# Kernel tuning notes

Hardware: AMD Instinct MI355X
Metric: run time of the kernel (lower is better)

## Reference

```python
import jax, jax.numpy as jnp
import numpy as np

N_NODES = 100000
N_EDGES = 1000000
N_GRAPHS = 2048
IN_DIM, HIDDEN, OUT_DIM = 5, 64, 128


def setup_inputs() -> dict:
    key = jax.random.key(0)
    ks = jax.random.split(key, 12)
    x = jax.random.normal(ks[0], (N_NODES, IN_DIM), dtype=jnp.float32)
    edge_index = jax.random.randint(ks[1], (2, N_EDGES), 0, N_NODES, dtype=jnp.int64)
    batch = jnp.sort(jax.random.randint(ks[2], (N_NODES,), 0, N_GRAPHS, dtype=jnp.int64))
    def lin(k, fan_in, fan_out):
        bound = 1.0 / np.sqrt(fan_in)
        kw, kb = jax.random.split(k)
        W = jax.random.uniform(kw, (fan_in, fan_out), jnp.float32, -bound, bound)
        b = jax.random.uniform(kb, (fan_out,), jnp.float32, -bound, bound)
        return W, b
    W1, b1 = lin(ks[3], IN_DIM, HIDDEN)
    W2, b2 = lin(ks[4], HIDDEN, HIDDEN)
    W3, b3 = lin(ks[5], HIDDEN, HIDDEN)
    W4, b4 = lin(ks[6], HIDDEN, OUT_DIM)
    return {"x": x, "edge_index": edge_index, "batch": batch,
            "W1": W1, "b1": b1, "W2": W2, "b2": b2,
            "W3": W3, "b3": b3, "W4": W4, "b4": b4}


def _gcn_conv(x, W, b, src, dst, norm, n):
    # h = x W; message from src, scaled by symmetric norm, scattered to dst
    h = x @ W                                   # [N, F]
    msg = h[src] * norm[:, None]                # [E+N, F] gather
    agg = jax.ops.segment_sum(msg, dst, num_segments=n)  # scatter-add
    return agg + b


def reference(x, edge_index, batch, W1, b1, W2, b2, W3, b3, W4, b4):
    n = x.shape[0]
    loop = jnp.arange(n, dtype=edge_index.dtype)
    # GCN with self-loops: src -> dst aggregation, D^-1/2 A_hat D^-1/2 norm
    src = jnp.concatenate([edge_index[0], loop])
    dst = jnp.concatenate([edge_index[1], loop])
    deg = jax.ops.segment_sum(jnp.ones_like(dst, dtype=x.dtype), dst, num_segments=n)
    dinv = jnp.where(deg > 0, jax.lax.rsqrt(jnp.maximum(deg, 1.0)), 0.0)
    norm = dinv[src] * dinv[dst]                # [E+N]

    h = jax.nn.relu(_gcn_conv(x, W1, b1, src, dst, norm, n))
    h = jax.nn.relu(_gcn_conv(h, W2, b2, src, dst, norm, n))

    # global mean pool per graph
    sums = jax.ops.segment_sum(h, batch, num_segments=N_GRAPHS)      # [G, F]
    cnts = jax.ops.segment_sum(jnp.ones((n,), h.dtype), batch, num_segments=N_GRAPHS)
    pooled = sums / jnp.maximum(cnts, 1.0)[:, None]

    # MLP head
    z = jax.nn.relu(pooled @ W3 + b3)
    return z @ W4 + b4
```

## Files before the change

kernel.cpp:

```cpp
#include <hip/hip_runtime.h>
#include <hip/hip_fp16.h>

#define N_NODES  100000
#define N_EDGES  1000000
#define N_GRAPHS 2048
#define IN_DIM   5
#define HIDDEN   64
#define OUT_DIM  128
#define CAP      32
#define NA       512
#define PART     256
#define NBIN     391
#define CAPBIN   4096
#define LSTR     72

typedef _Float16 f16x8 __attribute__((ext_vector_type(8)));
typedef float    f32x4 __attribute__((ext_vector_type(4)));


__global__ void __launch_bounds__(256) k_part2(
        const int* __restrict__ src, const int* __restrict__ dst,
        const int* __restrict__ batch, int* __restrict__ gcursor,
        int* __restrict__ epart, int* __restrict__ gs) {
    __shared__ int h[NBIN];
    __shared__ int off[NBIN];
    int t = threadIdx.x, b = blockIdx.x;

    int gid = b * 256 + t;
    if (gid < N_NODES) {
        int bi = batch[gid];
        int bp = (gid == 0) ? -1 : batch[gid - 1];
        for (int g = bp + 1; g <= bi; g++) gs[g] = gid;
        if (gid == N_NODES - 1)
            for (int g = bi + 1; g <= N_GRAPHS; g++) gs[g] = N_NODES;
    }

    for (int i = t; i < NBIN; i += 256) h[i] = 0;
    __syncthreads();
    for (int e = b * 256 + t; e < N_EDGES; e += NA * 256)
        atomicAdd(&h[dst[e] >> 8], 1);
    __syncthreads();
    for (int i = t; i < NBIN; i += 256) {
        int c = h[i];
        int base = c ? atomicAdd(&gcursor[i], c) : 0;
        off[i] = i * CAPBIN + base;
    }
    __syncthreads();
    for (int e = b * 256 + t; e < N_EDGES; e += NA * 256) {
        int d = dst[e];
        int bin = d >> 8;
        int pos = atomicAdd(&off[bin], 1);
        if (pos < (bin + 1) * CAPBIN)
            epart[pos] = ((d & (PART - 1)) << 17) | src[e];
    }
}

__global__ void __launch_bounds__(256) k_build(
        const int* __restrict__ epart, const int* __restrict__ bincnt,
        const float* __restrict__ x, int* __restrict__ cnt, int* __restrict__ bkt,
        float* __restrict__ dinv, __half* __restrict__ xs) {
    __shared__ int lcnt[PART];
    __shared__ int lrows[PART * CAP];
    int t = threadIdx.x, b = blockIdx.x;
    int base = b * PART;
    for (int i = t; i < PART; i += 256) lcnt[i] = 0;
    __syncthreads();
    int estart = b * CAPBIN;
    int eend = estart + min(bincnt[b], CAPBIN);
    for (int i = estart + t; i < eend; i += 256) {
        int ed = epart[i];
        int ln = ed >> 17;
        int c = atomicAdd(&lcnt[ln], 1);
        if (c < CAP) lrows[ln * CAP + c] = ed & 0x1FFFF;
    }
    __syncthreads();
    int gbase = base * CAP;
    int lim = min(PART * CAP, N_NODES * CAP - gbase);
    for (int i = t; i < lim; i += 256) bkt[gbase + i] = lrows[i];
    for (int n = t; n < PART; n += 256) {
        int g = base + n;
        if (g < N_NODES) {
            int c = lcnt[n];
            cnt[g] = c;
            float d = rsqrtf(1.0f + (float)c);
            dinv[g] = d;
            union { __half h[8]; float4 f4; } u;
#pragma unroll
            for (int k = 0; k < 8; k++)
                u.h[k] = __float2half((k < IN_DIM) ? x[g * IN_DIM + k] * d : 0.0f);
            ((float4*)xs)[g] = u.f4;
        }
    }
}

__global__ void __launch_bounds__(256) k_g5l12(
        const int* __restrict__ cnt, const int* __restrict__ bkt,
        const __half* __restrict__ xs,
        const float* __restrict__ W1, const float* __restrict__ b1,
        const float* __restrict__ W2, const float* __restrict__ dinv,
        __half* __restrict__ hs2h) {
    __shared__ _Float16 lh1[64 * LSTR];
    __shared__ _Float16 lw2[64 * LSTR];
    __shared__ float la5[64][8];
    int tid = threadIdx.x;
    int w = tid >> 6, l = tid & 63;
    int nodeBase = blockIdx.x * 64;

#pragma unroll
    for (int i = 0; i < 16; i++) {
        int idx = tid + i * 256;
        int k = idx >> 6, n = idx & 63;
        lw2[n * LSTR + k] = (_Float16)W2[k * HIDDEN + n];
    }

    {
        int g4 = l >> 2, l4 = l & 3;
        int ln = w * 16 + g4;
        int g = nodeBase + ln;
        float s0 = 0.f, s1 = 0.f, s2 = 0.f, s3 = 0.f;
        float s4 = 0.f, s5 = 0.f, s6 = 0.f, s7 = 0.f;
        if (g < N_NODES) {
            const float4* XS4 = (const float4*)xs;
            int len = min(cnt[g], CAP);
            const int* row = bkt + (size_t)g * CAP;
#define XACC(r) { const __half2* hp_ = (const __half2*)&(r);                   \
            float2 u0_ = __half22float2(hp_[0]), u1_ = __half22float2(hp_[1]); \
            float2 u2_ = __half22float2(hp_[2]), u3_ = __half22float2(hp_[3]); \
            s0 += u0_.x; s1 += u0_.y; s2 += u1_.x; s3 += u1_.y;                \
            s4 += u2_.x; s5 += u2_.y; s6 += u3_.x; s7 += u3_.y; }
            int e = l4;
            for (; e + 4 < len; e += 8) {
                float4 r0 = XS4[row[e]];
                float4 r1 = XS4[row[e + 4]];
                XACC(r0); XACC(r1);
            }
            if (e < len) { float4 r0 = XS4[row[e]]; XACC(r0); }
            if (l4 == 0) { float4 rs = XS4[g]; XACC(rs); }
#undef XACC
        }
#pragma unroll
        for (int m = 1; m <= 2; m <<= 1) {
            s0 += __shfl_xor(s0, m); s1 += __shfl_xor(s1, m);
            s2 += __shfl_xor(s2, m); s3 += __shfl_xor(s3, m);
            s4 += __shfl_xor(s4, m); s5 += __shfl_xor(s5, m);
            s6 += __shfl_xor(s6, m); s7 += __shfl_xor(s7, m);
        }
        if (l4 == 0) {
            float d = (g < N_NODES) ? dinv[g] : 0.f;
            la5[ln][0] = s0 * d; la5[ln][1] = s1 * d;
            la5[ln][2] = s2 * d; la5[ln][3] = s3 * d;
            la5[ln][4] = s4 * d; la5[ln][5] = s5 * d;
            la5[ln][6] = s6 * d; la5[ln][7] = s7 * d;
        }
    }

    int f = l;
    for (int i = 0; i < 16; i++) {
        int ln = w * 16 + i;
        float t1 = b1[f];
#pragma unroll
        for (int k = 0; k < IN_DIM; k++)
            t1 += la5[ln][k] * W1[k * HIDDEN + f];
        lh1[ln * LSTR + f] = (_Float16)fmaxf(t1, 0.f);
    }
    __syncthreads();

    int quad = l >> 4, m16 = l & 15;
    f32x4 acc0 = {0.f, 0.f, 0.f, 0.f};
    f32x4 acc1 = {0.f, 0.f, 0.f, 0.f};
    f32x4 acc2 = {0.f, 0.f, 0.f, 0.f};
    f32x4 acc3 = {0.f, 0.f, 0.f, 0.f};
#pragma unroll
    for (int kc = 0; kc < 2; kc++) {
        f16x8 a = *(const f16x8*)&lh1[(w * 16 + m16) * LSTR + kc * 32 + quad * 8];
        f16x8 b0 = *(const f16x8*)&lw2[(0 * 16 + m16) * LSTR + kc * 32 + quad * 8];
        f16x8 b1f = *(const f16x8*)&lw2[(1 * 16 + m16) * LSTR + kc * 32 + quad * 8];
        f16x8 b2 = *(const f16x8*)&lw2[(2 * 16 + m16) * LSTR + kc * 32 + quad * 8];
        f16x8 b3 = *(const f16x8*)&lw2[(3 * 16 + m16) * LSTR + kc * 32 + quad * 8];
        acc0 = __builtin_amdgcn_mfma_f32_16x16x32_f16(a, b0, acc0, 0, 0, 0);
        acc1 = __builtin_amdgcn_mfma_f32_16x16x32_f16(a, b1f, acc1, 0, 0, 0);
        acc2 = __builtin_amdgcn_mfma_f32_16x16x32_f16(a, b2, acc2, 0, 0, 0);
        acc3 = __builtin_amdgcn_mfma_f32_16x16x32_f16(a, b3, acc3, 0, 0, 0);
    }
#pragma unroll
    for (int i = 0; i < 4; i++) {
        int g = nodeBase + w * 16 + quad * 4 + i;
        if (g >= N_NODES) continue;
        float dv = dinv[g];
        __half* row = hs2h + (size_t)g * HIDDEN + m16;
        row[0]  = __float2half(acc0[i] * dv);
        row[16] = __float2half(acc1[i] * dv);
        row[32] = __float2half(acc2[i] * dv);
        row[48] = __float2half(acc3[i] * dv);
    }
}

__global__ void __launch_bounds__(256) k_g2ph(
        const int* __restrict__ cnt, const int* __restrict__ bkt,
        const __half* __restrict__ hs2h, const float* __restrict__ dinv,
        const int* __restrict__ gs, const float* __restrict__ b2,
        const float* __restrict__ W3, const float* __restrict__ b3,
        const float* __restrict__ W4, const float* __restrict__ b4,
        float* __restrict__ out) {
    __shared__ float pool[4][HIDDEN];
    __shared__ float gp[HIDDEN];
    __shared__ float gz[HIDDEN];
    int g = blockIdx.x, tid = threadIdx.x;
    int grp = tid >> 3, l8 = tid & 7;
    int w = tid >> 6;
    int s = gs[g], e = gs[g + 1];
    const float4* H16 = (const float4*)hs2h;
    float4 b2a = ((const float4*)b2)[l8 * 2];
    float4 b2b = ((const float4*)b2)[l8 * 2 + 1];
    float p0 = 0.f, p1 = 0.f, p2 = 0.f, p3 = 0.f;
    float p4 = 0.f, p5 = 0.f, p6 = 0.f, p7 = 0.f;

#define ACCA(r) { const __half2* hp_ = (const __half2*)&(r);               \
        float2 u0_ = __half22float2(hp_[0]), u1_ = __half22float2(hp_[1]); \
        float2 u2_ = __half22float2(hp_[2]), u3_ = __half22float2(hp_[3]); \
        a0 += u0_.x; a1 += u0_.y; a2 += u1_.x; a3 += u1_.y;                \
        a4 += u2_.x; a5 += u2_.y; a6 += u3_.x; a7 += u3_.y; }
#define ACCC(r) { const __half2* hp_ = (const __half2*)&(r);               \
        float2 u0_ = __half22float2(hp_[0]), u1_ = __half22float2(hp_[1]); \
        float2 u2_ = __half22float2(hp_[2]), u3_ = __half22float2(hp_[3]); \
        c0 += u0_.x; c1 += u0_.y; c2 += u1_.x; c3 += u1_.y;                \
        c4 += u2_.x; c5 += u2_.y; c6 += u3_.x; c7 += u3_.y; }

    for (int node = s + grp; node < e; node += 32) {
        int len = min(cnt[node], CAP);
        const int* row = bkt + (size_t)node * CAP;
        float a0 = 0.f, a1 = 0.f, a2 = 0.f, a3 = 0.f;
        float a4 = 0.f, a5 = 0.f, a6 = 0.f, a7 = 0.f;
        float c0 = 0.f, c1 = 0.f, c2 = 0.f, c3 = 0.f;
        float c4 = 0.f, c5 = 0.f, c6 = 0.f, c7 = 0.f;
        int ee = 0;
        for (; ee + 8 <= len; ee += 8) {
            int4 i0 = *(const int4*)&row[ee];
            int4 i1 = *(const int4*)&row[ee + 4];
            float4 r0 = H16[(size_t)i0.x * 8 + l8];
            float4 r1 = H16[(size_t)i0.y * 8 + l8];
            float4 r2 = H16[(size_t)i0.z * 8 + l8];
            float4 r3 = H16[(size_t)i0.w * 8 + l8];
            float4 r4 = H16[(size_t)i1.x * 8 + l8];
            float4 r5 = H16[(size_t)i1.y * 8 + l8];
            float4 r6 = H16[(size_t)i1.z * 8 + l8];
            float4 r7 = H16[(size_t)i1.w * 8 + l8];
            ACCA(r0); ACCC(r1); ACCA(r2); ACCC(r3);
            ACCA(r4); ACCC(r5); ACCA(r6); ACCC(r7);
        }
        if (ee + 4 <= len) {
            int4 i0 = *(const int4*)&row[ee];
            float4 r0 = H16[(size_t)i0.x * 8 + l8];
            float4 r1 = H16[(size_t)i0.y * 8 + l8];
            float4 r2 = H16[(size_t)i0.z * 8 + l8];
            float4 r3 = H16[(size_t)i0.w * 8 + l8];
            ACCA(r0); ACCC(r1); ACCA(r2); ACCC(r3);
            ee += 4;
        }
        for (; ee < len; ee++) {
            float4 r0 = H16[(size_t)row[ee] * 8 + l8];
            ACCA(r0);
        }
        {
            float4 rs = H16[(size_t)node * 8 + l8];
            ACCA(rs);
        }
        float d = dinv[node];
        p0 += fmaxf((a0 + c0) * d + b2a.x, 0.f);
        p1 += fmaxf((a1 + c1) * d + b2a.y, 0.f);
        p2 += fmaxf((a2 + c2) * d + b2a.z, 0.f);
        p3 += fmaxf((a3 + c3) * d + b2a.w, 0.f);
        p4 += fmaxf((a4 + c4) * d + b2b.x, 0.f);
        p5 += fmaxf((a5 + c5) * d + b2b.y, 0.f);
        p6 += fmaxf((a6 + c6) * d + b2b.z, 0.f);
        p7 += fmaxf((a7 + c7) * d + b2b.w, 0.f);
    }
#undef ACCA
#undef ACCC
#pragma unroll
    for (int m = 8; m <= 32; m <<= 1) {
        p0 += __shfl_xor(p0, m); p1 += __shfl_xor(p1, m);
        p2 += __shfl_xor(p2, m); p3 += __shfl_xor(p3, m);
        p4 += __shfl_xor(p4, m); p5 += __shfl_xor(p5, m);
        p6 += __shfl_xor(p6, m); p7 += __shfl_xor(p7, m);
    }
    if ((tid & 63) < 8) {
        float* pw = &pool[w][l8 * 8];
        pw[0] = p0; pw[1] = p1; pw[2] = p2; pw[3] = p3;
        pw[4] = p4; pw[5] = p5; pw[6] = p6; pw[7] = p7;
    }
    __syncthreads();
    if (tid < HIDDEN) {
        float inv = 1.0f / fmaxf((float)(e - s), 1.0f);
        gp[tid] = (pool[0][tid] + pool[1][tid] + pool[2][tid] + pool[3][tid]) * inv;
    }
    __syncthreads();
    if (tid < HIDDEN) {
        float t = b3[tid];
#pragma unroll 8
        for (int k = 0; k < HIDDEN; k++) t += gp[k] * W3[k * HIDDEN + tid];
        gz[tid] = fmaxf(t, 0.f);
    }
    __syncthreads();
    if (tid < OUT_DIM) {
        float t = b4[tid];
#pragma unroll 8
        for (int k = 0; k < HIDDEN; k++) t += gz[k] * W4[k * OUT_DIM + tid];
        out[(size_t)g * OUT_DIM + tid] = t;
    }
}

extern "C" void kernel_launch(void* const* d_in, const int* in_sizes, int n_in,
                              void* d_out, int out_size, void* d_ws, size_t ws_size,
                              hipStream_t stream) {
    const float* x  = (const float*)d_in[0];
    const int*   ei = (const int*)d_in[1];
    const int*   batch = (const int*)d_in[2];
    const float* W1 = (const float*)d_in[3];
    const float* b1 = (const float*)d_in[4];
    const float* W2 = (const float*)d_in[5];
    const float* b2 = (const float*)d_in[6];
    const float* W3 = (const float*)d_in[7];
    const float* b3 = (const float*)d_in[8];
    const float* W4 = (const float*)d_in[9];
    const float* b4 = (const float*)d_in[10];
    float* out = (float*)d_out;

    const int* src = ei;
    const int* dst = ei + N_EDGES;

    char* wp = (char*)d_ws;
    auto carve = [&](size_t bytes) -> void* {
        void* p = (void*)wp;
        wp += (bytes + 255) & ~(size_t)255;
        return p;
    };
    int*    cnt     = (int*)carve((size_t)N_NODES * sizeof(int));
    int*    bkt     = (int*)carve((size_t)N_NODES * CAP * sizeof(int));
    float*  dinv    = (float*)carve((size_t)N_NODES * sizeof(float));
    __half* hs2h    = (__half*)carve((size_t)N_NODES * HIDDEN * sizeof(__half));
    __half* xs      = (__half*)carve((size_t)N_NODES * 8 * sizeof(__half));
    int*    epart   = (int*)carve((size_t)NBIN * CAPBIN * sizeof(int));
    int*    gs      = (int*)carve((size_t)(N_GRAPHS + 1) * sizeof(int));
    int*    gcursor = (int*)carve((size_t)NBIN * sizeof(int));

    hipMemsetAsync(gcursor, 0, (size_t)NBIN * sizeof(int), stream);
    k_part2<<<NA, 256, 0, stream>>>(src, dst, batch, gcursor, epart, gs);
    k_build<<<NBIN, 256, 0, stream>>>(epart, gcursor, x, cnt, bkt, dinv, xs);
    k_g5l12<<<(N_NODES + 63) / 64, 256, 0, stream>>>(cnt, bkt, xs, W1, b1, W2,
                                                     dinv, hs2h);
    k_g2ph<<<N_GRAPHS, 256, 0, stream>>>(cnt, bkt, hs2h, dinv, gs, b2,
                                         W3, b3, W4, b4, out);
}
```

Before: 167.9 us.

## Sort nodes by degree per block and cache edge payloads in registers during partitioning

```diff
diff --git a/kernel.cpp b/kernel.cpp
--- a/kernel.cpp
+++ b/kernel.cpp
@@ -13,6 +13,8 @@
 #define NBIN     391
 #define CAPBIN   4096
 #define LSTR     72
+#define MAXN     192
+#define EPT      8
 
 typedef _Float16 f16x8 __attribute__((ext_vector_type(8)));
 typedef float    f32x4 __attribute__((ext_vector_type(4)));
@@ -37,8 +39,19 @@
 
     for (int i = t; i < NBIN; i += 256) h[i] = 0;
     __syncthreads();
-    for (int e = b * 256 + t; e < N_EDGES; e += NA * 256)
-        atomicAdd(&h[dst[e] >> 8], 1);
+    int ebin[EPT], epay[EPT];
+    int ebase = b * 256 + t;
+#pragma unroll
+    for (int i = 0; i < EPT; i++) {
+        int e = ebase + i * (NA * 256);
+        ebin[i] = -1;
+        if (e < N_EDGES) {
+            int d = dst[e];
+            ebin[i] = d >> 8;
+            epay[i] = ((d & (PART - 1)) << 17) | src[e];
+            atomicAdd(&h[ebin[i]], 1);
+        }
+    }
     __syncthreads();
     for (int i = t; i < NBIN; i += 256) {
         int c = h[i];
@@ -46,12 +59,13 @@
         off[i] = i * CAPBIN + base;
     }
     __syncthreads();
-    for (int e = b * 256 + t; e < N_EDGES; e += NA * 256) {
-        int d = dst[e];
-        int bin = d >> 8;
-        int pos = atomicAdd(&off[bin], 1);
-        if (pos < (bin + 1) * CAPBIN)
-            epart[pos] = ((d & (PART - 1)) << 17) | src[e];
+#pragma unroll
+    for (int i = 0; i < EPT; i++) {
+        if (ebin[i] >= 0) {
+            int pos = atomicAdd(&off[ebin[i]], 1);
+            if (pos < (ebin[i] + 1) * CAPBIN)
+                epart[pos] = epay[i];
+        }
     }
 }
 
@@ -102,6 +116,8 @@
     __shared__ _Float16 lh1[64 * LSTR];
     __shared__ _Float16 lw2[64 * LSTR];
     __shared__ float la5[64][8];
+    __shared__ unsigned short ordn[64];
+    __shared__ int dsh[CAP + 1];
     int tid = threadIdx.x;
     int w = tid >> 6, l = tid & 63;
     int nodeBase = blockIdx.x * 64;
@@ -113,10 +129,27 @@
         lw2[n * LSTR + k] = (_Float16)W2[k * HIDDEN + n];
     }
 
+    if (tid <= CAP) dsh[tid] = 0;
+    __syncthreads();
+    int mydeg = 0;
+    if (tid < 64) {
+        int g = nodeBase + tid;
+        mydeg = (g < N_NODES) ? min(cnt[g], CAP) : 0;
+        atomicAdd(&dsh[mydeg], 1);
+    }
+    __syncthreads();
+    if (tid == 0) {
+        int acc = 0;
+        for (int i = 0; i <= CAP; i++) { int c = dsh[i]; dsh[i] = acc; acc += c; }
+    }
+    __syncthreads();
+    if (tid < 64) { int pos = atomicAdd(&dsh[mydeg], 1); ordn[pos] = tid; }
+    __syncthreads();
+
     {
         int g4 = l >> 2, l4 = l & 3;
-        int ln = w * 16 + g4;
-        int g = nodeBase + ln;
+        int lnm = ordn[w * 16 + g4];
+        int g = nodeBase + lnm;
         float s0 = 0.f, s1 = 0.f, s2 = 0.f, s3 = 0.f;
         float s4 = 0.f, s5 = 0.f, s6 = 0.f, s7 = 0.f;
         if (g < N_NODES) {
@@ -147,12 +180,13 @@
         }
         if (l4 == 0) {
             float d = (g < N_NODES) ? dinv[g] : 0.f;
-            la5[ln][0] = s0 * d; la5[ln][1] = s1 * d;
-            la5[ln][2] = s2 * d; la5[ln][3] = s3 * d;
-            la5[ln][4] = s4 * d; la5[ln][5] = s5 * d;
-            la5[ln][6] = s6 * d; la5[ln][7] = s7 * d;
-        }
-    }
+            la5[lnm][0] = s0 * d; la5[lnm][1] = s1 * d;
+            la5[lnm][2] = s2 * d; la5[lnm][3] = s3 * d;
+            la5[lnm][4] = s4 * d; la5[lnm][5] = s5 * d;
+            la5[lnm][6] = s6 * d; la5[lnm][7] = s7 * d;
+        }
+    }
+    __syncthreads();
 
     int f = l;
     for (int i = 0; i < 16; i++) {
@@ -205,10 +239,31 @@
     __shared__ float pool[4][HIDDEN];
     __shared__ float gp[HIDDEN];
     __shared__ float gz[HIDDEN];
+    __shared__ unsigned short ord[MAXN];
+    __shared__ int dsh[CAP + 1];
     int g = blockIdx.x, tid = threadIdx.x;
     int grp = tid >> 3, l8 = tid & 7;
     int w = tid >> 6;
     int s = gs[g], e = gs[g + 1];
+    int n = e - s;
+    bool dosort = (n <= MAXN);
+
+    if (tid <= CAP) dsh[tid] = 0;
+    __syncthreads();
+    int mydeg = 0;
+    if (dosort && tid < n) {
+        mydeg = min(cnt[s + tid], CAP);
+        atomicAdd(&dsh[mydeg], 1);
+    }
+    __syncthreads();
+    if (tid == 0) {
+        int acc = 0;
+        for (int i = 0; i <= CAP; i++) { int c = dsh[i]; dsh[i] = acc; acc += c; }
+    }
+    __syncthreads();
+    if (dosort && tid < n) { int pos = atomicAdd(&dsh[mydeg], 1); ord[pos] = tid; }
+    __syncthreads();
+
     const float4* H16 = (const float4*)hs2h;
     float4 b2a = ((const float4*)b2)[l8 * 2];
     float4 b2b = ((const float4*)b2)[l8 * 2 + 1];
@@ -226,7 +281,8 @@
         c0 += u0_.x; c1 += u0_.y; c2 += u1_.x; c3 += u1_.y;                \
         c4 += u2_.x; c5 += u2_.y; c6 += u3_.x; c7 += u3_.y; }
 
-    for (int node = s + grp; node < e; node += 32) {
+    for (int r = grp; r < n; r += 32) {
+        int node = s + (dosort ? (int)ord[r] : r);
         int len = min(cnt[node], CAP);
         const int* row = bkt + (size_t)node * CAP;
         float a0 = 0.f, a1 = 0.f, a2 = 0.f, a3 = 0.f;
@@ -291,7 +347,7 @@
     }
     __syncthreads();
     if (tid < HIDDEN) {
-        float inv = 1.0f / fmaxf((float)(e - s), 1.0f);
+        float inv = 1.0f / fmaxf((float)n, 1.0f);
         gp[tid] = (pool[0][tid] + pool[1][tid] + pool[2][tid] + pool[3][tid]) * inv;
     }
     __syncthreads();
```

Result: faster. 163.3 us (-2.7%).
